# Optimization experiments

Measured on AMD Instinct MI355X. Metric: run time of the kernel, lower is better.

Reference implementation:

```python
import jax, jax.numpy as jnp
import numpy as np
import math

B, L = 4, 5
C, H, W = 256, 128, 256
REC_LEN = np.array([5, 4, 3, 2], dtype=np.int64)  # sum = 14
DOWNSAMPLE_RATE = 4.0
DISCRETE_RATIO = 0.4  # voxel_size[0]


def _make_t_matrix(key):
    k1, k2 = jax.random.split(key)
    theta = jax.random.uniform(k1, (B, L, L), minval=-0.05, maxval=0.05)
    trans = jax.random.uniform(k2, (B, L, L, 2), minval=-2.0, maxval=2.0)
    M = jnp.zeros((B, L, L, 4, 4), dtype=jnp.float32)
    M = M.at[..., 0, 0].set(jnp.cos(theta))
    M = M.at[..., 0, 1].set(-jnp.sin(theta))
    M = M.at[..., 1, 0].set(jnp.sin(theta))
    M = M.at[..., 1, 1].set(jnp.cos(theta))
    M = M.at[..., 2, 2].set(1.0)
    M = M.at[..., 3, 3].set(1.0)
    M = M.at[..., 0, 3].set(trans[..., 0])
    M = M.at[..., 1, 3].set(trans[..., 1])
    # ego->ego is identity
    eye = jnp.eye(4, dtype=jnp.float32)
    idx = jnp.arange(L)
    M = M.at[:, idx, idx].set(eye)
    return M


def setup_inputs() -> dict:
    key = jax.random.key(0)
    k1, k2, k3 = jax.random.split(key, 3)
    x = jax.random.normal(k1, (int(REC_LEN.sum()), C, H, W), dtype=jnp.float32)
    rm = jax.random.uniform(k2, (int(REC_LEN.sum()), 1, H, W), dtype=jnp.float32)
    pairwise_t_matrix = _make_t_matrix(k3)
    record_len = jnp.asarray(REC_LEN)
    return {"x": x, "rm": rm, "record_len": record_len,
            "pairwise_t_matrix": pairwise_t_matrix}


def warp_affine_simple(src, M):
    """src: (N,C,H,W), M: (N,2,3) normalized affine (torch affine_grid/grid_sample,
    align_corners=True, zero padding)."""
    N, Cc, Hh, Ww = src.shape
    ys = jnp.linspace(-1.0, 1.0, Hh, dtype=src.dtype)
    xs = jnp.linspace(-1.0, 1.0, Ww, dtype=src.dtype)
    gy, gx = jnp.meshgrid(ys, xs, indexing='ij')           # (H,W)
    base = jnp.stack([gx, gy, jnp.ones_like(gx)], axis=-1)  # (H,W,3)
    coords = jnp.einsum('nij,hwj->nhwi', M, base)           # (N,H,W,2) = (x', y')
    px = (coords[..., 0] + 1.0) * 0.5 * (Ww - 1)
    py = (coords[..., 1] + 1.0) * 0.5 * (Hh - 1)
    x0 = jnp.floor(px); y0 = jnp.floor(py)
    wx = px - x0; wy = py - y0

    def gather(xi, yi):
        valid = (xi >= 0) & (xi <= Ww - 1) & (yi >= 0) & (yi <= Hh - 1)
        xc = jnp.clip(xi, 0, Ww - 1).astype(jnp.int32)
        yc = jnp.clip(yi, 0, Hh - 1).astype(jnp.int32)
        v = jax.vmap(lambda s, y, x: s[:, y, x])(src, yc, xc)  # (N,C,H,W)
        return v * valid[:, None, :, :].astype(src.dtype)

    v00 = gather(x0, y0)
    v01 = gather(x0 + 1, y0)
    v10 = gather(x0, y0 + 1)
    v11 = gather(x0 + 1, y0 + 1)
    wx = wx[:, None]; wy = wy[:, None]  # (N,1,H,W)
    return (v00 * (1 - wx) * (1 - wy) + v01 * wx * (1 - wy)
            + v10 * (1 - wx) * wy + v11 * wx * wy)


def _forward(x, rm, pairwise_t_matrix, rl):
    _, Cc, Hh, Ww = x.shape
    # normalize 4x4 -> 2x3 affine in [-1,1] grid coords
    t = pairwise_t_matrix[:, :, :, (0, 1), :][:, :, :, :, (0, 1, 3)]  # (B,L,L,2,3)
    t = t.at[..., 0, 1].multiply(Hh / Ww)
    t = t.at[..., 1, 0].multiply(Ww / Hh)
    t = t.at[..., 0, 2].multiply(2.0 / (DOWNSAMPLE_RATE * DISCRETE_RATIO * Ww))
    t = t.at[..., 1, 2].multiply(2.0 / (DOWNSAMPLE_RATE * DISCRETE_RATIO * Hh))

    starts = np.concatenate([[0], np.cumsum(rl)[:-1]])
    inv_sqrt_c = 1.0 / math.sqrt(Cc)
    outs = []
    for b in range(len(rl)):  # ragged loop over small fixed batch
        N = int(rl[b]); s = int(starts[b])
        node = x[s:s + N]                       # (N,C,H,W)
        warped = warp_affine_simple(node, t[b, 0, :N])
        feat = warped.reshape(N, Cc, Hh * Ww).transpose(2, 0, 1)  # (HW,N,C)
        scores = jnp.einsum('pic,pjc->pij', feat, feat) * inv_sqrt_c
        attn = jax.nn.softmax(scores, axis=-1)
        ego = jnp.einsum('pij,pjc->pic', attn, feat)[:, 0, :]     # (HW,C)
        outs.append(ego.T.reshape(Cc, Hh, Ww))
    return jnp.stack(outs)  # (B,C,H,W)


def reference(x, rm, record_len, pairwise_t_matrix):
    rl = np.asarray(record_len)
    return _forward(x, rm, pairwise_t_matrix, rl)
```

## Files before the change

### kernel.cpp

```cpp
#include <hip/hip_runtime.h>
#include <hip/hip_bf16.h>
#include <math.h>

namespace {
constexpr int Cc = 256;
constexpr int Hh = 128;
constexpr int Ww = 256;
constexpr int HW  = Hh * Ww;
constexpr int CHW = Cc * HW;
constexpr int P     = 32;
constexpr int NTHR  = 512;
constexpr int CPG   = 16;
constexpr int TILES = HW / P;
}

struct alignas(4) F2 { float x, y; };

__device__ __forceinline__ unsigned short f2bf(float f) {
    __hip_bfloat16 h = __float2bfloat16(f);
    return __builtin_bit_cast(unsigned short, h);
}
__device__ __forceinline__ float bf2f(unsigned short u) {
    return __uint_as_float(((unsigned int)u) << 16);
}


template<int N>
__device__ __forceinline__ void run_body(const float* __restrict__ x,
                                         const float* __restrict__ tmat,
                                         float* __restrict__ out,
                                         int b, int tile, int tid,
                                         ushort4 (*feat)[P + 1],
                                         float (*dl)[5][P])
{
    constexpr int A = N - 1;
    const int lane = tid & 63;
    const int wv   = tid >> 6;
    const int pix  = lane & (P - 1);
    const int sub  = lane >> 5;
    const int g    = wv * 2 + sub;
    const int cbase = g * CPG;

    const int p = tile * P + pix;
    const int h = p >> 8;
    const int w = p & (Ww - 1);
    const int s = 5 * b - (b * (b - 1)) / 2;

    const float gx = -1.0f + 2.0f * (float)w / (float)(Ww - 1);
    const float gy = -1.0f + 2.0f * (float)h / (float)(Hh - 1);

    int   offp[A];
    float wxA[A], wxB[A], wyA[A], wyB[A];
#pragma unroll
    for (int a = 0; a < A; ++a) {
        const int j = a + 1;
        const float* Mp = tmat + (size_t)(b * 25 + j) * 16;
        const float a00 = Mp[0];
        const float a01 = Mp[1] * ((float)Hh / (float)Ww);
        const float a02 = Mp[3] * (2.0f / (4.0f * 0.4f * (float)Ww));
        const float a10 = Mp[4] * ((float)Ww / (float)Hh);
        const float a11 = Mp[5];
        const float a12 = Mp[7] * (2.0f / (4.0f * 0.4f * (float)Hh));
        const float px = (a00 * gx + a01 * gy + a02 + 1.0f) * 0.5f * (float)(Ww - 1);
        const float py = (a10 * gx + a11 * gy + a12 + 1.0f) * 0.5f * (float)(Hh - 1);
        const float x0f = floorf(px), y0f = floorf(py);
        const float fx = px - x0f, fy = py - y0f;
        const int x0 = (int)x0f, y0 = (int)y0f;
        const int xc = min(max(x0, 0), Ww - 2);
        const int yc = min(max(y0, 0), Hh - 2);
        const bool xin = (x0 >= 0) & (x0 <= Ww - 2);
        const bool yin = (y0 >= 0) & (y0 <= Hh - 2);
        wxA[a] = xin ? (1.f - fx) : ((x0 == -1)     ? fx         : 0.f);
        wxB[a] = xin ? fx         : ((x0 == Ww - 1) ? (1.f - fx) : 0.f);
        wyA[a] = yin ? (1.f - fy) : ((y0 == -1)     ? fy         : 0.f);
        wyB[a] = yin ? fy         : ((y0 == Hh - 1) ? (1.f - fy) : 0.f);
        offp[a] = yc * Ww + xc;
    }

    const float* xb0 = x + (size_t)s * CHW;

    float f0[CPG];
    float dj[5] = {0.f, 0.f, 0.f, 0.f, 0.f};
#pragma unroll
    for (int k = 0; k < CPG; ++k) {
        const float* pc = xb0 + (size_t)(cbase + k) * HW;
        const float v0 = pc[p];
        f0[k] = v0;
        dj[0] = fmaf(v0, v0, dj[0]);
        unsigned short pk[4] = {0, 0, 0, 0};
#pragma unroll
        for (int a = 0; a < A; ++a) {
            const float* q = pc + (size_t)(a + 1) * CHW + offp[a];
            const F2 r0 = *(const F2*)q;
            const F2 r1 = *(const F2*)(q + Ww);
            const float v = wyA[a] * (wxA[a] * r0.x + wxB[a] * r0.y)
                          + wyB[a] * (wxA[a] * r1.x + wxB[a] * r1.y);
            dj[a + 1] = fmaf(v0, v, dj[a + 1]);
            pk[a] = f2bf(v);
        }
        ushort4 u4; u4.x = pk[0]; u4.y = pk[1]; u4.z = pk[2]; u4.w = pk[3];
        feat[cbase + k][pix] = u4;
    }

#pragma unroll
    for (int j = 0; j < N; ++j) dj[j] += __shfl_xor(dj[j], 32);
    if (sub == 0) {
#pragma unroll
        for (int j = 0; j < N; ++j) dl[wv][j][pix] = dj[j];
    }
    __syncthreads();

    float e[5] = {0.f, 0.f, 0.f, 0.f, 0.f};
    {
        float sc[N];
#pragma unroll
        for (int j = 0; j < N; ++j) {
            float t = 0.f;
#pragma unroll
            for (int wvi = 0; wvi < 8; ++wvi) t += dl[wvi][j][pix];
            sc[j] = t * (1.0f / 16.0f);
        }
        float m = sc[0];
#pragma unroll
        for (int j = 1; j < N; ++j) m = fmaxf(m, sc[j]);
        float sum = 0.f;
#pragma unroll
        for (int j = 0; j < N; ++j) { e[j] = __expf(sc[j] - m); sum += e[j]; }
        const float inv = 1.0f / sum;
#pragma unroll
        for (int j = 0; j < N; ++j) e[j] *= inv;
    }

    float* ob = out + (size_t)b * CHW + p;
#pragma unroll
    for (int k = 0; k < CPG; ++k) {
        const ushort4 u = feat[cbase + k][pix];
        float acc = e[0] * f0[k];
        if constexpr (N > 1) acc = fmaf(e[1], bf2f(u.x), acc);
        if constexpr (N > 2) acc = fmaf(e[2], bf2f(u.y), acc);
        if constexpr (N > 3) acc = fmaf(e[3], bf2f(u.z), acc);
        if constexpr (N > 4) acc = fmaf(e[4], bf2f(u.w), acc);
        __builtin_nontemporal_store(acc, ob + (size_t)(cbase + k) * HW);
    }
}

__global__ __launch_bounds__(NTHR, 4)
void atten_fused(const float* __restrict__ x,
                 const float* __restrict__ tmat,
                 float* __restrict__ out)
{
    __shared__ ushort4 feat[Cc][P + 1];
    __shared__ float   dl[8][5][P];

    const int b    = blockIdx.x >> 10;
    const int tile = blockIdx.x & (TILES - 1);
    const int tid  = threadIdx.x;

    if      (b == 0) run_body<5>(x, tmat, out, 0, tile, tid, feat, dl);
    else if (b == 1) run_body<4>(x, tmat, out, 1, tile, tid, feat, dl);
    else if (b == 2) run_body<3>(x, tmat, out, 2, tile, tid, feat, dl);
    else             run_body<2>(x, tmat, out, 3, tile, tid, feat, dl);
}

extern "C" void kernel_launch(void* const* d_in, const int* in_sizes, int n_in,
                              void* d_out, int out_size, void* d_ws, size_t ws_size,
                              hipStream_t stream) {
    const float* x    = (const float*)d_in[0];
    const float* tmat = (const float*)d_in[3];
    float* out = (float*)d_out;
    dim3 grid(4 * TILES);
    dim3 block(NTHR);
    hipLaunchKernelGGL(atten_fused, grid, block, 0, stream, x, tmat, out);
}
```

Measured before the change: 195.6 us.

## Keep warped bf16 features in registers and widen tile to 64 pixels

Each thread now keeps its packed bf16 warped neighbor features in registers instead of staging them in a shared-memory feature tile. The tile grows to 64 pixels with 1024 threads, so each wave covers a full 64-lane pixel row and the cross-half shuffle reduction is dropped. This removes the LDS round trip and most of the LDS footprint. In exchange it raises register pressure, with launch bounds of 1024 threads and 4 blocks, and doubles the number of waves per block that meet at the barrier.

```diff
diff --git a/kernel.cpp b/kernel.cpp
--- a/kernel.cpp
+++ b/kernel.cpp
@@ -8,8 +8,8 @@
 constexpr int Ww = 256;
 constexpr int HW  = Hh * Ww;
 constexpr int CHW = Cc * HW;
-constexpr int P     = 32;
-constexpr int NTHR  = 512;
+constexpr int P     = 64;
+constexpr int NTHR  = 1024;
 constexpr int CPG   = 16;
 constexpr int TILES = HW / P;
 }
@@ -30,18 +30,14 @@
                                          const float* __restrict__ tmat,
                                          float* __restrict__ out,
                                          int b, int tile, int tid,
-                                         ushort4 (*feat)[P + 1],
                                          float (*dl)[5][P])
 {
     constexpr int A = N - 1;
     const int lane = tid & 63;
     const int wv   = tid >> 6;
-    const int pix  = lane & (P - 1);
-    const int sub  = lane >> 5;
-    const int g    = wv * 2 + sub;
-    const int cbase = g * CPG;
+    const int cbase = wv * CPG;
 
-    const int p = tile * P + pix;
+    const int p = tile * P + lane;
     const int h = p >> 8;
     const int w = p & (Ww - 1);
     const int s = 5 * b - (b * (b - 1)) / 2;
@@ -80,6 +76,8 @@
     const float* xb0 = x + (size_t)s * CHW;
 
     float f0[CPG];
+    unsigned fe0[CPG];
+    unsigned fe1[(A > 2) ? CPG : 1];
     float dj[5] = {0.f, 0.f, 0.f, 0.f, 0.f};
 #pragma unroll
     for (int k = 0; k < CPG; ++k) {
@@ -98,16 +96,12 @@
             dj[a + 1] = fmaf(v0, v, dj[a + 1]);
             pk[a] = f2bf(v);
         }
-        ushort4 u4; u4.x = pk[0]; u4.y = pk[1]; u4.z = pk[2]; u4.w = pk[3];
-        feat[cbase + k][pix] = u4;
+        fe0[k] = (unsigned)pk[0] | ((unsigned)pk[1] << 16);
+        if constexpr (A > 2) fe1[k] = (unsigned)pk[2] | ((unsigned)pk[3] << 16);
     }
 
 #pragma unroll
-    for (int j = 0; j < N; ++j) dj[j] += __shfl_xor(dj[j], 32);
-    if (sub == 0) {
-#pragma unroll
-        for (int j = 0; j < N; ++j) dl[wv][j][pix] = dj[j];
-    }
+    for (int j = 0; j < N; ++j) dl[wv][j][lane] = dj[j];
     __syncthreads();
 
     float e[5] = {0.f, 0.f, 0.f, 0.f, 0.f};
@@ -117,7 +111,7 @@
         for (int j = 0; j < N; ++j) {
             float t = 0.f;
 #pragma unroll
-            for (int wvi = 0; wvi < 8; ++wvi) t += dl[wvi][j][pix];
+            for (int wvi = 0; wvi < 16; ++wvi) t += dl[wvi][j][lane];
             sc[j] = t * (1.0f / 16.0f);
         }
         float m = sc[0];
@@ -134,12 +128,16 @@
     float* ob = out + (size_t)b * CHW + p;
 #pragma unroll
     for (int k = 0; k < CPG; ++k) {
-        const ushort4 u = feat[cbase + k][pix];
         float acc = e[0] * f0[k];
-        if constexpr (N > 1) acc = fmaf(e[1], bf2f(u.x), acc);
-        if constexpr (N > 2) acc = fmaf(e[2], bf2f(u.y), acc);
-        if constexpr (N > 3) acc = fmaf(e[3], bf2f(u.z), acc);
-        if constexpr (N > 4) acc = fmaf(e[4], bf2f(u.w), acc);
+        const unsigned u0 = fe0[k];
+        acc = fmaf(e[1], bf2f((unsigned short)(u0 & 0xffffu)), acc);
+        if constexpr (A > 1) acc = fmaf(e[2], bf2f((unsigned short)(u0 >> 16)), acc);
+        if constexpr (A > 2) {
+            const unsigned u1 = fe1[k];
+            acc = fmaf(e[3], bf2f((unsigned short)(u1 & 0xffffu)), acc);
+            if constexpr (A > 3)
+                acc = fmaf(e[4], bf2f((unsigned short)(u1 >> 16)), acc);
+        }
         __builtin_nontemporal_store(acc, ob + (size_t)(cbase + k) * HW);
     }
 }
@@ -149,17 +147,16 @@
                  const float* __restrict__ tmat,
                  float* __restrict__ out)
 {
-    __shared__ ushort4 feat[Cc][P + 1];
-    __shared__ float   dl[8][5][P];
+    __shared__ float dl[16][5][P];
 
-    const int b    = blockIdx.x >> 10;
+    const int b    = blockIdx.x >> 9;
     const int tile = blockIdx.x & (TILES - 1);
     const int tid  = threadIdx.x;
 
-    if      (b == 0) run_body<5>(x, tmat, out, 0, tile, tid, feat, dl);
-    else if (b == 1) run_body<4>(x, tmat, out, 1, tile, tid, feat, dl);
-    else if (b == 2) run_body<3>(x, tmat, out, 2, tile, tid, feat, dl);
-    else             run_body<2>(x, tmat, out, 3, tile, tid, feat, dl);
+    if      (b == 0) run_body<5>(x, tmat, out, 0, tile, tid, dl);
+    else if (b == 1) run_body<4>(x, tmat, out, 1, tile, tid, dl);
+    else if (b == 2) run_body<3>(x, tmat, out, 2, tile, tid, dl);
+    else             run_body<2>(x, tmat, out, 3, tile, tid, dl);
 }
 
 extern "C" void kernel_launch(void* const* d_in, const int* in_sizes, int n_in,
```

Result: slower. 247.9 us (+26.7%).
